# Performance work log

Hardware: AMD Instinct MI355X
Metric: run time of the kernel (lower is better)

## Reference

```python
import jax, jax.numpy as jnp
import numpy as np

N_NODES = 50000
N_EDGES = 800000
N_GRAPHS = 256
IN_DIM, HIDDEN_DIM, EMBED_DIM = 128, 64, 128


def setup_inputs() -> dict:
    key = jax.random.key(0)
    ks = jax.random.split(key, 8)
    x = jax.random.normal(ks[0], (N_NODES, IN_DIM), dtype=jnp.float32)
    edge_index = jax.random.randint(ks[1], (2, N_EDGES), 0, N_NODES, dtype=jnp.int64)
    edge_weight = jax.random.uniform(ks[2], (N_EDGES,), dtype=jnp.float32)
    batch_vec = jnp.sort(jax.random.randint(ks[3], (N_NODES,), 0, N_GRAPHS, dtype=jnp.int64))
    # Glorot-ish params for the two GCNConv layers
    W1 = jax.random.normal(ks[4], (IN_DIM, HIDDEN_DIM), dtype=jnp.float32) / np.sqrt(IN_DIM)
    b1 = jnp.zeros((HIDDEN_DIM,), dtype=jnp.float32)
    W2 = jax.random.normal(ks[5], (HIDDEN_DIM, EMBED_DIM), dtype=jnp.float32) / np.sqrt(HIDDEN_DIM)
    b2 = jnp.zeros((EMBED_DIM,), dtype=jnp.float32)
    return {"x": x, "edge_index": edge_index, "edge_weight": edge_weight,
            "batch_vec": batch_vec, "W1": W1, "b1": b1, "W2": W2, "b2": b2}


def _gcn_conv(x, src, dst, ew, W, b, num_nodes):
    # PyG GCNConv: linear transform, add self-loops (weight 1), sym-normalize, aggregate at dst.
    h = x @ W  # [N, out]
    loops = jnp.arange(num_nodes, dtype=src.dtype)
    row = jnp.concatenate([src, loops])
    col = jnp.concatenate([dst, loops])
    w = jnp.concatenate([ew, jnp.ones((num_nodes,), x.dtype)])
    deg = jax.ops.segment_sum(w, col, num_segments=num_nodes)
    dis = jnp.where(deg > 0, jax.lax.rsqrt(deg), 0.0)  # deg^{-1/2}, inf -> 0
    norm = dis[row] * w * dis[col]  # [E+N]
    msg = h[row] * norm[:, None]  # gather + scale
    out = jax.ops.segment_sum(msg, col, num_segments=num_nodes)  # scatter-add
    return out + b


def reference(x, edge_index, edge_weight, batch_vec, W1, b1, W2, b2):
    src, dst = edge_index[0], edge_index[1]
    h = jax.nn.relu(_gcn_conv(x, src, dst, edge_weight, W1, b1, N_NODES))
    # dropout is identity at inference
    h = jax.nn.relu(_gcn_conv(h, src, dst, edge_weight, W2, b2, N_NODES))
    # global_mean_pool over graphs
    s = jax.ops.segment_sum(h, batch_vec, num_segments=N_GRAPHS)
    cnt = jax.ops.segment_sum(jnp.ones((N_NODES,), h.dtype), batch_vec, num_segments=N_GRAPHS)
    return s / jnp.maximum(cnt, 1.0)[:, None]
```

## Files before the change

### kernel.cpp

```cpp
#include <hip/hip_runtime.h>

constexpr int N_NODES  = 50000;
constexpr int N_EDGES  = 800000;
constexpr int N_GRAPHS = 256;
constexpr int IN_DIM   = 128;
constexpr int HID      = 64;
constexpr int EMB      = 128;
constexpr int NBKT     = 196;
constexpr int EB       = (N_EDGES + 1023) / 1024;
constexpr int GB       = N_NODES / 16;
constexpr int GSB      = (N_NODES + 255) / 256;
constexpr int NB2      = 64;

constexpr size_t OFF_POOL  = 0;
constexpr size_t OFF_GST   = 32768;
constexpr size_t OFF_BBASE = 33026;
constexpr size_t OFF_DIS   = 33224;
constexpr size_t OFF_RS    = 83224;
constexpr size_t OFF_HCNT  = 133224;
constexpr size_t OFF_REC   = 286496;
constexpr size_t OFF_PART  = OFF_REC + 2 * (size_t)N_EDGES;
constexpr size_t OFF_H1    = OFF_PART;
constexpr size_t OFF_H1P   = OFF_PART + 4 * (size_t)N_EDGES;
constexpr size_t OFF_AGG2  = OFF_H1P;

__global__ __launch_bounds__(256) void k_p1(const int* __restrict__ dst,
                                            int* __restrict__ hcnt) {
    __shared__ int lh[NBKT];
    int tid = threadIdx.x;
    for (int i = tid; i < NBKT; i += 256) lh[i] = 0;
    __syncthreads();
    int base = blockIdx.x * 1024;
    #pragma unroll
    for (int j = 0; j < 4; ++j) {
        int e = base + j * 256 + tid;
        if (e < N_EDGES) atomicAdd(&lh[dst[e] >> 8], 1);
    }
    __syncthreads();
    for (int i = tid; i < NBKT; i += 256) hcnt[blockIdx.x * NBKT + i] = lh[i];
}

__global__ __launch_bounds__(256) void k_kab(const int* __restrict__ hcnt,
                                             int* __restrict__ bbase) {
    __shared__ int tile[256];
    int t = threadIdx.x;
    int v = 0;
    if (t < NBKT) {
        for (int i = 0; i < EB; ++i) v += hcnt[i * NBKT + t];
    }
    tile[t] = v;
    __syncthreads();
    for (int off = 1; off < 256; off <<= 1) {
        int a = (t >= off) ? tile[t - off] : 0;
        __syncthreads();
        tile[t] += a;
        __syncthreads();
    }
    if (t < NBKT) bbase[t] = tile[t] - v;
    if (t == NBKT - 1) bbase[NBKT] = tile[t];
}

__global__ __launch_bounds__(256) void k_kc(int* __restrict__ hcnt,
                                            const int* __restrict__ bbase,
                                            const int* __restrict__ batch,
                                            int* __restrict__ gstart) {
    __shared__ int tile[256];
    __shared__ int carry;
    int t = threadIdx.x;
    if (blockIdx.x < NBKT) {
        int b = blockIdx.x;
        if (t == 0) carry = bbase[b];
        __syncthreads();
        for (int i0 = 0; i0 < EB; i0 += 256) {
            int i = i0 + t;
            int v = (i < EB) ? hcnt[i * NBKT + b] : 0;
            tile[t] = v;
            __syncthreads();
            for (int off = 1; off < 256; off <<= 1) {
                int a = (t >= off) ? tile[t - off] : 0;
                __syncthreads();
                tile[t] += a;
                __syncthreads();
            }
            int incl = tile[t];
            if (i < EB) hcnt[i * NBKT + b] = carry + incl - v;
            __syncthreads();
            if (t == 255) carry += incl;
            __syncthreads();
        }
        return;
    }
    int i = (blockIdx.x - NBKT) * 256 + t;
    if (i >= N_NODES) return;
    int g = batch[i];
    if (i == 0) {
        for (int gg = 0; gg <= g; ++gg) gstart[gg] = 0;
    } else {
        int gp = batch[i - 1];
        for (int gg = gp + 1; gg <= g; ++gg) gstart[gg] = i;
    }
    if (i == N_NODES - 1) {
        for (int gg = g + 1; gg <= N_GRAPHS; ++gg) gstart[gg] = N_NODES;
    }
}

__global__ __launch_bounds__(256) void k_p2(const int* __restrict__ src,
                                            const int* __restrict__ dst,
                                            const float* __restrict__ ew,
                                            const int* __restrict__ hcnt,
                                            uint4* __restrict__ part) {
    __shared__ int lb[NBKT];
    __shared__ int lc[NBKT];
    int tid = threadIdx.x;
    for (int i = tid; i < NBKT; i += 256) {
        lb[i] = hcnt[blockIdx.x * NBKT + i];
        lc[i] = 0;
    }
    __syncthreads();
    int base = blockIdx.x * 1024;
    #pragma unroll
    for (int j = 0; j < 4; ++j) {
        int e = base + j * 256 + tid;
        if (e < N_EDGES) {
            int d = dst[e];
            int b = d >> 8;
            int r = atomicAdd(&lc[b], 1);
            part[lb[b] + r] = make_uint4((unsigned)src[e], (unsigned)d,
                                         __float_as_uint(ew[e]), 0u);
        }
    }
}

__global__ __launch_bounds__(256) void k_p3_gemm1(const uint4* __restrict__ part,
                                                  const int* __restrict__ bbase,
                                                  int* __restrict__ rs,
                                                  float* __restrict__ dis,
                                                  uint2* __restrict__ rec,
                                                  const float* __restrict__ x,
                                                  const float* __restrict__ W1,
                                                  float* __restrict__ h) {
    __shared__ float Ws[IN_DIM * HID];
    __shared__ float xs[16][IN_DIM + 1];
    __shared__ int   cnt[256];
    __shared__ float dgw[256];
    __shared__ int   scn[256];
    __shared__ int   cur[256];
    int tid = threadIdx.x;
    if (blockIdx.x < NBKT) {
        int b = blockIdx.x;
        int base_node = b << 8;
        int ebeg = bbase[b], eend = bbase[b + 1];
        cnt[tid] = 0;
        dgw[tid] = 0.f;
        __syncthreads();
        for (int e = ebeg + tid; e < eend; e += 256) {
            uint4 r = part[e];
            int ld = (int)r.y & 255;
            atomicAdd(&cnt[ld], 1);
            atomicAdd(&dgw[ld], __uint_as_float(r.z));
        }
        __syncthreads();
        scn[tid] = cnt[tid];
        __syncthreads();
        for (int off = 1; off < 256; off <<= 1) {
            int a = (tid >= off) ? scn[tid - off] : 0;
            __syncthreads();
            scn[tid] += a;
            __syncthreads();
        }
        int node = base_node + tid;
        if (node < N_NODES) {
            rs[node] = ebeg + scn[tid];
            dis[node] = rsqrtf(dgw[tid] + 1.0f);
        }
        cur[tid] = ebeg + scn[tid] - cnt[tid];
        __syncthreads();
        for (int e = ebeg + tid; e < eend; e += 256) {
            uint4 r = part[e];
            int ld = (int)r.y & 255;
            int pos = atomicAdd(&cur[ld], 1);
            rec[pos] = make_uint2(r.x, r.z);
        }
        return;
    }
    int bid = blockIdx.x - NBKT;
    const float4* W4 = (const float4*)W1;
    float4* Ws4 = (float4*)Ws;
    for (int i = tid; i < IN_DIM * HID / 4; i += 256) Ws4[i] = W4[i];
    int base = bid * 16;
    for (int i = tid; i < 16 * IN_DIM; i += 256) {
        int ln = i >> 7, k = i & 127;
        xs[ln][k] = x[(size_t)(base + ln) * IN_DIM + k];
    }
    __syncthreads();
    int ln = tid >> 4;
    int jc = (tid & 15) * 4;
    float4 acc = make_float4(0.f, 0.f, 0.f, 0.f);
    #pragma unroll 4
    for (int k = 0; k < IN_DIM; ++k) {
        float a = xs[ln][k];
        float4 w = *(const float4*)&Ws[k * HID + jc];
        acc.x += a * w.x; acc.y += a * w.y; acc.z += a * w.z; acc.w += a * w.w;
    }
    *(float4*)&h[(size_t)(base + ln) * HID + jc] = acc;
}

template <bool RELU_BIAS>
__global__ __launch_bounds__(256) void k_gather64(const uint2* __restrict__ rec,
                                                  const int* __restrict__ rs,
                                                  const float* __restrict__ dis,
                                                  const float* __restrict__ T,
                                                  const float* __restrict__ bias,
                                                  float* __restrict__ out) {
    int wave = (blockIdx.x * 256 + threadIdx.x) >> 6;
    int lane = threadIdx.x & 63;
    int half = lane >> 5;
    int l    = lane & 31;
    if (wave >= N_NODES) return;
    int n = wave;
    int begin = (n == 0) ? 0 : rs[n - 1];
    int end = rs[n];
    const float2* T2 = (const float2*)T;

    float ax0 = 0.f, ay0 = 0.f, ax1 = 0.f, ay1 = 0.f;
    float ax2 = 0.f, ay2 = 0.f, ax3 = 0.f, ay3 = 0.f;
    int k = begin + half;
    while (k + 6 < end) {
        uint2 r0 = rec[k];
        uint2 r1 = rec[k + 2];
        uint2 r2 = rec[k + 4];
        uint2 r3 = rec[k + 6];
        float d0 = dis[r0.x];
        float d1 = dis[r1.x];
        float d2 = dis[r2.x];
        float d3 = dis[r3.x];
        float2 t0 = T2[(size_t)r0.x * 32 + l];
        float2 t1 = T2[(size_t)r1.x * 32 + l];
        float2 t2 = T2[(size_t)r2.x * 32 + l];
        float2 t3 = T2[(size_t)r3.x * 32 + l];
        float n0 = d0 * __uint_as_float(r0.y);
        float n1 = d1 * __uint_as_float(r1.y);
        float n2 = d2 * __uint_as_float(r2.y);
        float n3 = d3 * __uint_as_float(r3.y);
        ax0 += t0.x * n0; ay0 += t0.y * n0;
        ax1 += t1.x * n1; ay1 += t1.y * n1;
        ax2 += t2.x * n2; ay2 += t2.y * n2;
        ax3 += t3.x * n3; ay3 += t3.y * n3;
        k += 8;
    }
    while (k < end) {
        uint2 r = rec[k];
        float nn = dis[r.x] * __uint_as_float(r.y);
        float2 t = T2[(size_t)r.x * 32 + l];
        ax0 += t.x * nn; ay0 += t.y * nn;
        k += 2;
    }
    float ax = (ax0 + ax1) + (ax2 + ax3);
    float ay = (ay0 + ay1) + (ay2 + ay3);
    float di = dis[n];
    if (half == 0) {
        float2 t = T2[(size_t)n * 32 + l];
        ax += t.x * di; ay += t.y * di;
    }
    ax += __shfl_xor(ax, 32, 64);
    ay += __shfl_xor(ay, 32, 64);
    if (half == 0) {
        ax *= di; ay *= di;
        if (RELU_BIAS) {
            const float2* B2 = (const float2*)bias;
            float2 b = B2[l];
            ax += b.x; ay += b.y;
            ax = ax > 0.f ? ax : 0.f;
            ay = ay > 0.f ? ay : 0.f;
        }
        ((float2*)out)[(size_t)n * 32 + l] = make_float2(ax, ay);
    }
}

__global__ __launch_bounds__(256) void k_gemm2_pool(const float* __restrict__ agg,
                                                    const float* __restrict__ W2,
                                                    const float* __restrict__ b2,
                                                    const int* __restrict__ batch,
                                                    float* __restrict__ pool) {
    __shared__ float Ws[HID * EMB];
    __shared__ float as[NB2][HID];
    __shared__ int   bs[NB2];
    int tid = threadIdx.x;
    const float4* W4 = (const float4*)W2;
    float4* Ws4 = (float4*)Ws;
    for (int i = tid; i < HID * EMB / 4; i += 256) Ws4[i] = W4[i];
    int base = blockIdx.x * NB2;
    const float4* A4 = (const float4*)agg;
    float4* as4 = (float4*)as;
    for (int i = tid; i < NB2 * HID / 4; i += 256) {
        int node = base + (i >> 4);
        as4[i] = (node < N_NODES) ? A4[(size_t)node * 16 + (i & 15)]
                                  : make_float4(0.f, 0.f, 0.f, 0.f);
    }
    if (tid < NB2) {
        int node = base + tid;
        bs[tid] = (node < N_NODES) ? batch[node] : -1;
    }
    __syncthreads();

    int c = tid & 31;
    int s = tid >> 5;
    int jc = c * 4;
    float4 bq = *(const float4*)&b2[jc];
    float4 racc = make_float4(0.f, 0.f, 0.f, 0.f);
    int gcur = -1;
    for (int ni = s * 8; ni < s * 8 + 8; ++ni) {
        int g = bs[ni];
        if (g != gcur) {
            if (gcur >= 0) {
                float* p = &pool[(size_t)gcur * EMB + jc];
                atomicAdd(p + 0, racc.x); atomicAdd(p + 1, racc.y);
                atomicAdd(p + 2, racc.z); atomicAdd(p + 3, racc.w);
            }
            racc = make_float4(0.f, 0.f, 0.f, 0.f);
            gcur = g;
        }
        if (g < 0) continue;
        float4 acc = bq;
        #pragma unroll 8
        for (int k = 0; k < HID; ++k) {
            float a = as[ni][k];
            float4 w = Ws4[k * 32 + c];
            acc.x += a * w.x; acc.y += a * w.y; acc.z += a * w.z; acc.w += a * w.w;
        }
        racc.x += fmaxf(acc.x, 0.f);
        racc.y += fmaxf(acc.y, 0.f);
        racc.z += fmaxf(acc.z, 0.f);
        racc.w += fmaxf(acc.w, 0.f);
    }
    if (gcur >= 0) {
        float* p = &pool[(size_t)gcur * EMB + jc];
        atomicAdd(p + 0, racc.x); atomicAdd(p + 1, racc.y);
        atomicAdd(p + 2, racc.z); atomicAdd(p + 3, racc.w);
    }
}

__global__ void k_divide(const float* __restrict__ pool, const int* __restrict__ gstart,
                         float* __restrict__ out) {
    int idx = blockIdx.x * blockDim.x + threadIdx.x;
    if (idx >= N_GRAPHS * EMB) return;
    int g = idx >> 7;
    float c = (float)(gstart[g + 1] - gstart[g]);
    out[idx] = pool[idx] / fmaxf(c, 1.0f);
}

extern "C" void kernel_launch(void* const* d_in, const int* in_sizes, int n_in,
                              void* d_out, int out_size, void* d_ws, size_t ws_size,
                              hipStream_t stream) {
    const float* x     = (const float*)d_in[0];
    const int*   eidx  = (const int*)d_in[1];
    const float* ew    = (const float*)d_in[2];
    const int*   batch = (const int*)d_in[3];
    const float* W1    = (const float*)d_in[4];
    const float* b1    = (const float*)d_in[5];
    const float* W2    = (const float*)d_in[6];
    const float* b2    = (const float*)d_in[7];
    float* out = (float*)d_out;

    const int* src = eidx;
    const int* dst = eidx + N_EDGES;

    float* ws     = (float*)d_ws;
    float* pool   = ws + OFF_POOL;
    int*   gstart = (int*)(ws + OFF_GST);
    int*   bbase  = (int*)(ws + OFF_BBASE);
    float* dis    = ws + OFF_DIS;
    int*   rs     = (int*)(ws + OFF_RS);
    int*   hcnt   = (int*)(ws + OFF_HCNT);
    uint2* rec    = (uint2*)(ws + OFF_REC);
    uint4* part   = (uint4*)(ws + OFF_PART);
    float* h1     = ws + OFF_H1;
    float* h1p    = ws + OFF_H1P;
    float* agg2   = ws + OFF_AGG2;

    hipMemsetAsync(pool, 0, (size_t)N_GRAPHS * EMB * sizeof(float), stream);

    k_p1<<<EB, 256, 0, stream>>>(dst, hcnt);
    k_kab<<<1, 256, 0, stream>>>(hcnt, bbase);
    k_kc<<<NBKT + GSB, 256, 0, stream>>>(hcnt, bbase, batch, gstart);
    k_p2<<<EB, 256, 0, stream>>>(src, dst, ew, hcnt, part);

    k_p3_gemm1<<<NBKT + GB, 256, 0, stream>>>(part, bbase, rs, dis, rec, x, W1, h1p);

    k_gather64<true><<<N_NODES / 4, 256, 0, stream>>>(rec, rs, dis, h1p, b1, h1);

    k_gather64<false><<<N_NODES / 4, 256, 0, stream>>>(rec, rs, dis, h1, nullptr, agg2);

    k_gemm2_pool<<<(N_NODES + NB2 - 1) / NB2, 256, 0, stream>>>(agg2, W2, b2, batch, pool);

    k_divide<<<(N_GRAPHS * EMB + 255) / 256, 256, 0, stream>>>(pool, gstart, out);
}
```

Baseline: 281.2 us.

## Store intermediate node features in bf16 and widen GEMM1 to two nodes per thread

The hidden features h1p and h1 are now stored as packed bf16 pairs and expanded to fp32 inside the gather kernels. This halves the bytes fetched by the random per-edge gathers, which are expected to dominate the aggregation cost. GEMM1 also changes to 32 nodes per block with float4 loads and two nodes per thread, so each W load is reused twice. Accuracy drops because the stored intermediates carry only bf16 precision.

```diff
diff --git a/kernel.cpp b/kernel.cpp
--- a/kernel.cpp
+++ b/kernel.cpp
@@ -8,7 +8,7 @@
 constexpr int EMB      = 128;
 constexpr int NBKT     = 196;
 constexpr int EB       = (N_EDGES + 1023) / 1024;
-constexpr int GB       = N_NODES / 16;
+constexpr int GB       = (N_NODES + 31) / 32;
 constexpr int GSB      = (N_NODES + 255) / 256;
 constexpr int NB2      = 64;
 
@@ -23,6 +23,20 @@
 constexpr size_t OFF_H1    = OFF_PART;
 constexpr size_t OFF_H1P   = OFF_PART + 4 * (size_t)N_EDGES;
 constexpr size_t OFF_AGG2  = OFF_H1P;
+
+__device__ inline unsigned bf16r(float f) {
+    unsigned u = __float_as_uint(f);
+    return (u + 0x7fffu + ((u >> 16) & 1u)) >> 16;
+}
+__device__ inline unsigned bf16pack2(float lo, float hi) {
+    return bf16r(lo) | (bf16r(hi) << 16);
+}
+__device__ inline float bflo(unsigned v) { return __uint_as_float(v << 16); }
+__device__ inline float bfhi(unsigned v) { return __uint_as_float(v & 0xffff0000u); }
+
+__device__ inline void fma4(float4& acc, float s, const float4& v) {
+    acc.x += s * v.x; acc.y += s * v.y; acc.z += s * v.z; acc.w += s * v.w;
+}
 
 __global__ __launch_bounds__(256) void k_p1(const int* __restrict__ dst,
                                             int* __restrict__ hcnt) {
@@ -138,9 +152,9 @@
                                                   uint2* __restrict__ rec,
                                                   const float* __restrict__ x,
                                                   const float* __restrict__ W1,
-                                                  float* __restrict__ h) {
+                                                  unsigned* __restrict__ h) {
     __shared__ float Ws[IN_DIM * HID];
-    __shared__ float xs[16][IN_DIM + 1];
+    __shared__ float xs[32][IN_DIM + 4];
     __shared__ int   cnt[256];
     __shared__ float dgw[256];
     __shared__ int   scn[256];
@@ -187,31 +201,50 @@
     const float4* W4 = (const float4*)W1;
     float4* Ws4 = (float4*)Ws;
     for (int i = tid; i < IN_DIM * HID / 4; i += 256) Ws4[i] = W4[i];
-    int base = bid * 16;
-    for (int i = tid; i < 16 * IN_DIM; i += 256) {
-        int ln = i >> 7, k = i & 127;
-        xs[ln][k] = x[(size_t)(base + ln) * IN_DIM + k];
-    }
-    __syncthreads();
-    int ln = tid >> 4;
-    int jc = (tid & 15) * 4;
-    float4 acc = make_float4(0.f, 0.f, 0.f, 0.f);
+    int base = bid * 32;
+    const float4* X4 = (const float4*)x;
+    for (int i = tid; i < 32 * 32; i += 256) {
+        int ln = i >> 5, kq = i & 31;
+        int node = base + ln;
+        float4 v = (node < N_NODES) ? X4[(size_t)node * 32 + kq]
+                                    : make_float4(0.f, 0.f, 0.f, 0.f);
+        *(float4*)&xs[ln][kq * 4] = v;
+    }
+    __syncthreads();
+    int np = tid >> 4;
+    int q  = tid & 15;
+    int n0 = np * 2, n1 = n0 + 1;
+    float4 a0 = make_float4(0.f, 0.f, 0.f, 0.f);
+    float4 a1 = a0;
     #pragma unroll 4
-    for (int k = 0; k < IN_DIM; ++k) {
-        float a = xs[ln][k];
-        float4 w = *(const float4*)&Ws[k * HID + jc];
-        acc.x += a * w.x; acc.y += a * w.y; acc.z += a * w.z; acc.w += a * w.w;
-    }
-    *(float4*)&h[(size_t)(base + ln) * HID + jc] = acc;
-}
-
-template <bool RELU_BIAS>
+    for (int k4 = 0; k4 < IN_DIM; k4 += 4) {
+        float4 xv0 = *(const float4*)&xs[n0][k4];
+        float4 xv1 = *(const float4*)&xs[n1][k4];
+        float4 w0 = Ws4[(k4 + 0) * 16 + q];
+        float4 w1 = Ws4[(k4 + 1) * 16 + q];
+        float4 w2 = Ws4[(k4 + 2) * 16 + q];
+        float4 w3 = Ws4[(k4 + 3) * 16 + q];
+        fma4(a0, xv0.x, w0); fma4(a0, xv0.y, w1); fma4(a0, xv0.z, w2); fma4(a0, xv0.w, w3);
+        fma4(a1, xv1.x, w0); fma4(a1, xv1.y, w1); fma4(a1, xv1.z, w2); fma4(a1, xv1.w, w3);
+    }
+    int nd0 = base + n0, nd1 = base + n1;
+    if (nd0 < N_NODES) {
+        uint2 p = make_uint2(bf16pack2(a0.x, a0.y), bf16pack2(a0.z, a0.w));
+        ((uint2*)h)[(size_t)nd0 * 16 + q] = p;
+    }
+    if (nd1 < N_NODES) {
+        uint2 p = make_uint2(bf16pack2(a1.x, a1.y), bf16pack2(a1.z, a1.w));
+        ((uint2*)h)[(size_t)nd1 * 16 + q] = p;
+    }
+}
+
+template <bool RELU_BIAS, bool OUT_BF16>
 __global__ __launch_bounds__(256) void k_gather64(const uint2* __restrict__ rec,
                                                   const int* __restrict__ rs,
                                                   const float* __restrict__ dis,
-                                                  const float* __restrict__ T,
+                                                  const unsigned* __restrict__ T,
                                                   const float* __restrict__ bias,
-                                                  float* __restrict__ out) {
+                                                  void* __restrict__ outv) {
     int wave = (blockIdx.x * 256 + threadIdx.x) >> 6;
     int lane = threadIdx.x & 63;
     int half = lane >> 5;
@@ -220,7 +253,6 @@
     int n = wave;
     int begin = (n == 0) ? 0 : rs[n - 1];
     int end = rs[n];
-    const float2* T2 = (const float2*)T;
 
     float ax0 = 0.f, ay0 = 0.f, ax1 = 0.f, ay1 = 0.f;
     float ax2 = 0.f, ay2 = 0.f, ax3 = 0.f, ay3 = 0.f;
@@ -234,33 +266,33 @@
         float d1 = dis[r1.x];
         float d2 = dis[r2.x];
         float d3 = dis[r3.x];
-        float2 t0 = T2[(size_t)r0.x * 32 + l];
-        float2 t1 = T2[(size_t)r1.x * 32 + l];
-        float2 t2 = T2[(size_t)r2.x * 32 + l];
-        float2 t3 = T2[(size_t)r3.x * 32 + l];
+        unsigned t0 = T[(size_t)r0.x * 32 + l];
+        unsigned t1 = T[(size_t)r1.x * 32 + l];
+        unsigned t2 = T[(size_t)r2.x * 32 + l];
+        unsigned t3 = T[(size_t)r3.x * 32 + l];
         float n0 = d0 * __uint_as_float(r0.y);
         float n1 = d1 * __uint_as_float(r1.y);
         float n2 = d2 * __uint_as_float(r2.y);
         float n3 = d3 * __uint_as_float(r3.y);
-        ax0 += t0.x * n0; ay0 += t0.y * n0;
-        ax1 += t1.x * n1; ay1 += t1.y * n1;
-        ax2 += t2.x * n2; ay2 += t2.y * n2;
-        ax3 += t3.x * n3; ay3 += t3.y * n3;
+        ax0 += bflo(t0) * n0; ay0 += bfhi(t0) * n0;
+        ax1 += bflo(t1) * n1; ay1 += bfhi(t1) * n1;
+        ax2 += bflo(t2) * n2; ay2 += bfhi(t2) * n2;
+        ax3 += bflo(t3) * n3; ay3 += bfhi(t3) * n3;
         k += 8;
     }
     while (k < end) {
         uint2 r = rec[k];
         float nn = dis[r.x] * __uint_as_float(r.y);
-        float2 t = T2[(size_t)r.x * 32 + l];
-        ax0 += t.x * nn; ay0 += t.y * nn;
+        unsigned t = T[(size_t)r.x * 32 + l];
+        ax0 += bflo(t) * nn; ay0 += bfhi(t) * nn;
         k += 2;
     }
     float ax = (ax0 + ax1) + (ax2 + ax3);
     float ay = (ay0 + ay1) + (ay2 + ay3);
     float di = dis[n];
     if (half == 0) {
-        float2 t = T2[(size_t)n * 32 + l];
-        ax += t.x * di; ay += t.y * di;
+        unsigned t = T[(size_t)n * 32 + l];
+        ax += bflo(t) * di; ay += bfhi(t) * di;
     }
     ax += __shfl_xor(ax, 32, 64);
     ay += __shfl_xor(ay, 32, 64);
@@ -273,7 +305,11 @@
             ax = ax > 0.f ? ax : 0.f;
             ay = ay > 0.f ? ay : 0.f;
         }
-        ((float2*)out)[(size_t)n * 32 + l] = make_float2(ax, ay);
+        if (OUT_BF16) {
+            ((unsigned*)outv)[(size_t)n * 32 + l] = bf16pack2(ax, ay);
+        } else {
+            ((float2*)outv)[(size_t)n * 32 + l] = make_float2(ax, ay);
+        }
     }
 }
 
@@ -374,11 +410,11 @@
     int*   hcnt   = (int*)(ws + OFF_HCNT);
     uint2* rec    = (uint2*)(ws + OFF_REC);
     uint4* part   = (uint4*)(ws + OFF_PART);
-    float* h1     = ws + OFF_H1;
-    float* h1p    = ws + OFF_H1P;
+    unsigned* h1  = (unsigned*)(ws + OFF_H1);
+    unsigned* h1p = (unsigned*)(ws + OFF_H1P);
     float* agg2   = ws + OFF_AGG2;
 
-    hipMemsetAsync(pool, 0, (size_t)N_GRAPHS * EMB * sizeof(float), stream);
+    (void)hipMemsetAsync(pool, 0, (size_t)N_GRAPHS * EMB * sizeof(float), stream);
 
     k_p1<<<EB, 256, 0, stream>>>(dst, hcnt);
     k_kab<<<1, 256, 0, stream>>>(hcnt, bbase);
@@ -387,9 +423,9 @@
 
     k_p3_gemm1<<<NBKT + GB, 256, 0, stream>>>(part, bbase, rs, dis, rec, x, W1, h1p);
 
-    k_gather64<true><<<N_NODES / 4, 256, 0, stream>>>(rec, rs, dis, h1p, b1, h1);
-
-    k_gather64<false><<<N_NODES / 4, 256, 0, stream>>>(rec, rs, dis, h1, nullptr, agg2);
+    k_gather64<true, true><<<N_NODES / 4, 256, 0, stream>>>(rec, rs, dis, h1p, b1, h1);
+
+    k_gather64<false, false><<<N_NODES / 4, 256, 0, stream>>>(rec, rs, dis, h1, nullptr, agg2);
 
     k_gemm2_pool<<<(N_NODES + NB2 - 1) / NB2, 256, 0, stream>>>(agg2, W2, b2, batch, pool);
 
```

Result: faster. 259.9 us (-7.5%).
